# Optimization experiments

Hardware: AMD Instinct MI355X
Metric: run time of the kernel (lower is better)

Reference implementation:

```python
import jax, jax.numpy as jnp
import numpy as np

B, H, W, C, NH = 4, 64, 64, 512, 16
HD = C // NH
BIAS_LEVEL = 0.1
LN_EPS = 1e-5


def layernorm(x, g, b):
    m = jnp.mean(x, axis=-1, keepdims=True)
    v = jnp.mean(jnp.square(x - m), axis=-1, keepdims=True)
    return (x - m) * jax.lax.rsqrt(v + LN_EPS) * g + b


def partition(x, idx):
    # x: [B, L, C] -> windows [nW, S, C]
    xg = x.reshape(B, H, W, C)
    if idx == 0:  # horizontal strips: window = one row of length W
        return xg.reshape(B * H, W, C)
    else:  # vertical strips: window = one column of length H, ordered by column
        return xg.transpose(0, 2, 1, 3).reshape(B * W, H, C)


def unpartition(w, idx):
    # w: [nW, S, C] -> [B, L, C]
    if idx == 0:
        return w.reshape(B, H * W, C)
    else:
        return w.reshape(B, W, H, C).transpose(0, 2, 1, 3).reshape(B, H * W, C)


def eg_attention(q, k, v, res_x, rpe, idx):
    # q,k,v: [B, L, C]; res_x: [B, L, C]; rpe: [1, NH, S, S]
    S = rpe.shape[-1]
    nW = (B * H * W) // S

    def to_heads(t):
        return partition(t, idx).reshape(nW, S, NH, HD).transpose(0, 2, 1, 3)

    qh, kh, vh = to_heads(q), to_heads(k), to_heads(v)  # [nW, NH, S, HD]
    attn = jnp.einsum('whsd,whtd->whst', qh, kh) + BIAS_LEVEL * rpe
    # gating mask from raw scores
    M = jnp.mean(jnp.abs(attn), axis=(1, 2, 3), keepdims=True)  # [nW,1,1,1]
    M = M / jnp.max(M)
    M = jnp.maximum(M, 0.5)
    # L2-normalize rows, trig transform
    norm = jnp.sqrt(jnp.sum(jnp.square(attn), axis=-1, keepdims=True))
    attn = attn / jnp.maximum(norm, 1e-12)
    attn = 1.0 - jnp.cos(attn * (jnp.pi / 2))
    attn = attn * M
    out = jnp.einsum('whst,whtd->whsd', attn, vh)  # [nW, NH, S, HD]
    out = out.transpose(0, 2, 1, 3).reshape(nW, S, C)
    out = unpartition(out, idx)  # [B, L, C]
    # masked residual: res_x is chunked sequentially (row-major), as in the source
    res = res_x.reshape(nW, S, C) * (1.0 - M[:, 0])
    res = res.reshape(B, H * W, C)
    return out + res


def eg_block(x, rpe, idx, ln1_g, ln1_b, wqkv, wproj, bproj, ln2_g, ln2_b,
             wfc1, bfc1, wfc2, bfc2):
    img = layernorm(x, ln1_g, ln1_b)
    qkv = img @ wqkv  # [B, L, 3C]
    q, k, v = jnp.split(qkv, 3, axis=-1)
    att = eg_attention(q, k, v, x, rpe, idx)
    att = att @ wproj + bproj
    x = x + att
    h = layernorm(x, ln2_g, ln2_b)
    h = jax.nn.gelu(h @ wfc1 + bfc1, approximate=False) @ wfc2 + bfc2
    return x + h


def setup_inputs() -> dict:
    key = jax.random.key(0)
    ks = jax.random.split(key, 16)
    d = {
        'x': jax.random.normal(ks[0], (B, H * W, C), jnp.float32),
        'rpe0': jax.random.normal(ks[1], (1, NH, W, W), jnp.float32),
        'rpe1': jax.random.normal(ks[2], (1, NH, H, H), jnp.float32),
    }
    for i, blk in enumerate(['0', '1']):
        kk = jax.random.split(ks[3 + i], 8)
        d['ln1_g' + blk] = jnp.ones((C,), jnp.float32)
        d['ln1_b' + blk] = jnp.zeros((C,), jnp.float32)
        d['wqkv' + blk] = jax.random.normal(kk[0], (C, 3 * C), jnp.float32) * 0.02
        d['wproj' + blk] = jax.random.normal(kk[1], (C, C), jnp.float32) * 0.02
        d['bproj' + blk] = jnp.zeros((C,), jnp.float32)
        d['ln2_g' + blk] = jnp.ones((C,), jnp.float32)
        d['ln2_b' + blk] = jnp.zeros((C,), jnp.float32)
        d['wfc1_' + blk] = jax.random.normal(kk[2], (C, 4 * C), jnp.float32) * 0.02
        d['bfc1_' + blk] = jnp.zeros((4 * C,), jnp.float32)
        d['wfc2_' + blk] = jax.random.normal(kk[3], (4 * C, C), jnp.float32) * 0.02
        d['bfc2_' + blk] = jnp.zeros((C,), jnp.float32)
    return d


def reference(x, rpe0, rpe1,
              ln1_g0, ln1_b0, wqkv0, wproj0, bproj0, ln2_g0, ln2_b0,
              wfc1_0, bfc1_0, wfc2_0, bfc2_0,
              ln1_g1, ln1_b1, wqkv1, wproj1, bproj1, ln2_g1, ln2_b1,
              wfc1_1, bfc1_1, wfc2_1, bfc2_1):
    x = eg_block(x, rpe0, 0, ln1_g0, ln1_b0, wqkv0, wproj0, bproj0,
                 ln2_g0, ln2_b0, wfc1_0, bfc1_0, wfc2_0, bfc2_0)
    x = eg_block(x, rpe1, 1, ln1_g1, ln1_b1, wqkv1, wproj1, bproj1,
                 ln2_g1, ln2_b1, wfc1_1, bfc1_1, wfc2_1, bfc2_1)
    return x
```

## Files before the change

### kernel.cpp

```cpp
#include <hip/hip_runtime.h>
#include <cstdint>
#include <cstddef>

typedef __bf16 bf16;
typedef __attribute__((ext_vector_type(4))) float f32x4;
typedef __attribute__((ext_vector_type(8))) __bf16 bf16x8;
typedef __attribute__((ext_vector_type(4))) __bf16 bf16x4;

static __device__ __forceinline__ f32x4 mfma16(bf16x8 a, bf16x8 b, f32x4 c) {
    return __builtin_amdgcn_mfma_f32_16x16x32_bf16(a, b, c, 0, 0, 0);
}

#define GLOAD_LDS16(gsrc, ldst)                                              \
    __builtin_amdgcn_global_load_lds(                                        \
        (const __attribute__((address_space(1))) void*)(gsrc),               \
        (__attribute__((address_space(3))) void*)(ldst), 16, 0, 0)

static __device__ __forceinline__ float fast_gelu(float x) {
    const float xs = x * 0.70710678118f;
    const float a  = fabsf(xs);
    const float t  = 1.0f / fmaf(0.3275911f, a, 1.0f);
    float p = fmaf(t, 1.061405429f, -1.453152027f);
    p = fmaf(t, p, 1.421413741f);
    p = fmaf(t, p, -0.284496736f);
    p = fmaf(t, p, 0.254829592f);
    const float erfa = 1.0f - p * t * __expf(-a * a);
    const float erfx = (xs < 0.f) ? -erfa : erfa;
    return 0.5f * x * (1.0f + erfx);
}

__global__ __launch_bounds__(256)
void transpose_cast(const float* __restrict__ W, bf16* __restrict__ Wt, int K, int N) {
    __shared__ float tile[32][33];
    const int n0 = blockIdx.x * 32, k0 = blockIdx.y * 32;
    const int tx = threadIdx.x & 31, ty = threadIdx.x >> 5;
    #pragma unroll
    for (int i = ty; i < 32; i += 8)
        tile[i][tx] = W[(size_t)(k0 + i) * N + n0 + tx];
    __syncthreads();
    #pragma unroll
    for (int i = ty; i < 32; i += 8)
        Wt[(size_t)(n0 + i) * K + k0 + tx] = (bf16)tile[tx][i];
}

__global__ __launch_bounds__(256)
void ln_kernel(const float* __restrict__ x, const float* __restrict__ g,
               const float* __restrict__ b, bf16* __restrict__ out) {
    const int row = blockIdx.x * 4 + (threadIdx.x >> 6);
    const int lane = threadIdx.x & 63;
    const float* p = x + (size_t)row * 512 + lane * 8;
    const float4 a0 = *(const float4*)p;
    const float4 a1 = *(const float4*)(p + 4);
    float vx[8] = {a0.x, a0.y, a0.z, a0.w, a1.x, a1.y, a1.z, a1.w};
    float s = 0.f, ss = 0.f;
    #pragma unroll
    for (int k = 0; k < 8; ++k) { s += vx[k]; ss += vx[k] * vx[k]; }
    #pragma unroll
    for (int m = 1; m < 64; m <<= 1) {
        s  += __shfl_xor(s, m);
        ss += __shfl_xor(ss, m);
    }
    const float mean = s * (1.0f / 512.0f);
    const float var  = ss * (1.0f / 512.0f) - mean * mean;
    const float inv  = rsqrtf(var + 1e-5f);
    const int c0 = lane * 8;
    const float4 g0 = *(const float4*)&g[c0], g1 = *(const float4*)&g[c0 + 4];
    const float4 b0 = *(const float4*)&b[c0], b1 = *(const float4*)&b[c0 + 4];
    const float gv[8] = {g0.x, g0.y, g0.z, g0.w, g1.x, g1.y, g1.z, g1.w};
    const float bv[8] = {b0.x, b0.y, b0.z, b0.w, b1.x, b1.y, b1.z, b1.w};
    bf16x8 o;
    #pragma unroll
    for (int k = 0; k < 8; ++k)
        o[k] = (bf16)((vx[k] - mean) * inv * gv[k] + bv[k]);
    *(bf16x8*)&out[(size_t)row * 512 + c0] = o;
}

template <int EPI>
__global__ __launch_bounds__(256)
void gemm_bt(const bf16* __restrict__ A, const bf16* __restrict__ Bt,
             int N, int K, const float* __restrict__ bias,
             const float* __restrict__ res, float* __restrict__ outf,
             bf16* __restrict__ outh) {
    __shared__ __align__(16) bf16 lsA[2][128 * 32];
    __shared__ __align__(16) bf16 lsB[2][128 * 32];
    const int nx = gridDim.x;
    const int nwg = nx * gridDim.y;
    const int flat = blockIdx.y * nx + blockIdx.x;
    const int cpx = nwg >> 3;
    const int bswz = (flat & 7) * cpx + (flat >> 3);
    const int bn = bswz % nx, bm = bswz / nx;

    const int tid = threadIdx.x, lane = tid & 63, wv = tid >> 6;
    const int wm = (wv & 1) * 64, wn = (wv >> 1) * 64;
    const int l15 = lane & 15, lg = lane >> 4;
    const size_t abase = (size_t)bm * 128 * K;
    const size_t bbase = (size_t)bn * 128 * K;
    const int srow = lane >> 2;
    const int slot = lane & 3;
    const int r0 = (wv * 2 + 0) * 16 + srow;
    const int r1 = (wv * 2 + 1) * 16 + srow;
    const int ks0 = (slot ^ ((r0 >> 1) & 3)) * 8;
    const int ks1 = (slot ^ ((r1 >> 1) & 3)) * 8;

    f32x4 acc[4][4] = {};

    auto stage = [&](int buf, int kt) {
        GLOAD_LDS16(&A[abase + (size_t)r0 * K + kt + ks0],
                    &lsA[buf][(wv * 2 + 0) * 512]);
        GLOAD_LDS16(&A[abase + (size_t)r1 * K + kt + ks1],
                    &lsA[buf][(wv * 2 + 1) * 512]);
        GLOAD_LDS16(&Bt[bbase + (size_t)r0 * K + kt + ks0],
                    &lsB[buf][(wv * 2 + 0) * 512]);
        GLOAD_LDS16(&Bt[bbase + (size_t)r1 * K + kt + ks1],
                    &lsB[buf][(wv * 2 + 1) * 512]);
    };
    auto compute = [&](int buf) {
        bf16x8 af[4], bfr[4];
        #pragma unroll
        for (int i = 0; i < 4; ++i) {
            const int r = wm + i * 16 + l15;
            af[i] = *(const bf16x8*)
                &lsA[buf][r * 32 + ((lg ^ ((r >> 1) & 3)) * 8)];
        }
        #pragma unroll
        for (int j = 0; j < 4; ++j) {
            const int r = wn + j * 16 + l15;
            bfr[j] = *(const bf16x8*)
                &lsB[buf][r * 32 + ((lg ^ ((r >> 1) & 3)) * 8)];
        }
        #pragma unroll
        for (int i = 0; i < 4; ++i)
            #pragma unroll
            for (int j = 0; j < 4; ++j)
                acc[i][j] = mfma16(af[i], bfr[j], acc[i][j]);
    };

    const int NK = K >> 5;
    stage(0, 0);
    __syncthreads();
    int cur = 0;
    for (int t = 0; t < NK - 1; ++t) {
        stage(cur ^ 1, (t + 1) * 32);
        compute(cur);
        __syncthreads();
        cur ^= 1;
    }
    compute(cur);

    #pragma unroll
    for (int i = 0; i < 4; ++i) {
        #pragma unroll
        for (int r = 0; r < 4; ++r) {
            const size_t row = (size_t)bm * 128 + wm + i * 16 + lg * 4 + r;
            #pragma unroll
            for (int j = 0; j < 4; ++j) {
                const int col = bn * 128 + wn + j * 16 + l15;
                const float v = acc[i][j][r];
                if constexpr (EPI == 0) {
                    outh[row * N + col] = (bf16)v;
                } else if constexpr (EPI == 1) {
                    outf[row * N + col] = v + bias[col] + res[row * N + col];
                } else {
                    outh[row * N + col] = (bf16)fast_gelu(v + bias[col]);
                }
            }
        }
    }
}

__global__ __launch_bounds__(256)
void attn_stats(const bf16* __restrict__ qkv, const float* __restrict__ rpe,
                float* __restrict__ Mraw4, int idx) {
    __shared__ float lsum[4];
    const int bid = blockIdx.x;
    const int w = bid >> 2;
    const int tid = threadIdx.x, lane = tid & 63, wv = tid >> 6;
    const int h = (bid & 3) * 4 + wv;
    const int l15 = lane & 15, lg = lane >> 4;
    const long gbase = (idx == 0) ? (long)w * 64 : ((long)(w >> 6) * 4096 + (w & 63));
    const long gstride = (idx == 0) ? 1 : 64;
    bf16x8 kf[4];
    #pragma unroll
    for (int i = 0; i < 4; ++i) {
        const long gs = gbase + (long)(i * 16 + l15) * gstride;
        kf[i] = *(const bf16x8*)&qkv[gs * 1536 + 512 + h * 32 + lg * 8];
    }
    const float* rh = rpe + h * 4096;
    float asum = 0.f;
    #pragma unroll
    for (int mi = 0; mi < 4; ++mi) {
        const long gs = gbase + (long)(mi * 16 + l15) * gstride;
        const bf16x8 qf = *(const bf16x8*)&qkv[gs * 1536 + h * 32 + lg * 8];
        f32x4 sc[4] = {};
        #pragma unroll
        for (int ni = 0; ni < 4; ++ni) sc[ni] = mfma16(qf, kf[ni], sc[ni]);
        #pragma unroll
        for (int r = 0; r < 4; ++r) {
            const int srow = mi * 16 + lg * 4 + r;
            #pragma unroll
            for (int ni = 0; ni < 4; ++ni)
                asum += fabsf(sc[ni][r] + 0.1f * rh[srow * 64 + ni * 16 + l15]);
        }
    }
    #pragma unroll
    for (int m = 1; m < 64; m <<= 1) asum += __shfl_xor(asum, m);
    if (lane == 0) lsum[wv] = asum;
    __syncthreads();
    if (tid == 0) Mraw4[bid] = lsum[0] + lsum[1] + lsum[2] + lsum[3];
}

__global__ __launch_bounds__(256)
void mcalc(const float* __restrict__ Mraw4, float* __restrict__ Mv) {
    __shared__ float red[4];
    const int t = threadIdx.x, lane = t & 63;
    const float v = (Mraw4[t * 4] + Mraw4[t * 4 + 1] + Mraw4[t * 4 + 2] +
                     Mraw4[t * 4 + 3]) * (1.0f / 65536.0f);
    float m = v;
    #pragma unroll
    for (int msk = 1; msk < 64; msk <<= 1) m = fmaxf(m, __shfl_xor(m, msk));
    if (lane == 0) red[t >> 6] = m;
    __syncthreads();
    const float mm = fmaxf(fmaxf(red[0], red[1]), fmaxf(red[2], red[3]));
    Mv[t] = fmaxf(v / mm, 0.5f);
}

__global__ __launch_bounds__(256)
void attn_apply(const bf16* __restrict__ qkv, const float* __restrict__ rpe,
                const float* __restrict__ Mv, const float* __restrict__ xin,
                bf16* __restrict__ attout, int idx) {
    __shared__ __align__(16) bf16 lsP[4][64 * 64];
    __shared__ __align__(16) bf16 lsVt[4][32 * 64];
    const int bid = blockIdx.x;
    const int w = bid >> 2;
    const int tid = threadIdx.x, lane = tid & 63, wv = tid >> 6;
    const int h = (bid & 3) * 4 + wv;
    const int l15 = lane & 15, lg = lane >> 4;
    const long gbase = (idx == 0) ? (long)w * 64 : ((long)(w >> 6) * 4096 + (w & 63));
    const long gstride = (idx == 0) ? 1 : 64;
    const float Mw = Mv[w];
    bf16* P  = lsP[wv];
    bf16* Vt = lsVt[wv];

    {
        const int d4 = (lane & 7) * 4;
        #pragma unroll
        for (int it = 0; it < 8; ++it) {
            const int t = it * 8 + (lane >> 3);
            const bf16x4 v = *(const bf16x4*)
                &qkv[(gbase + (long)t * gstride) * 1536 + 1024 + h * 32 + d4];
            #pragma unroll
            for (int e = 0; e < 4; ++e) {
                const int d = d4 + e;
                Vt[d * 64 + (t ^ ((d & 7) * 8))] = v[e];
            }
        }
    }
    bf16x8 kf[4];
    #pragma unroll
    for (int i = 0; i < 4; ++i) {
        const long gs = gbase + (long)(i * 16 + l15) * gstride;
        kf[i] = *(const bf16x8*)&qkv[gs * 1536 + 512 + h * 32 + lg * 8];
    }
    const float* rh = rpe + h * 4096;
    #pragma unroll
    for (int mi = 0; mi < 4; ++mi) {
        const long gs = gbase + (long)(mi * 16 + l15) * gstride;
        const bf16x8 qf = *(const bf16x8*)&qkv[gs * 1536 + h * 32 + lg * 8];
        f32x4 sc[4] = {};
        #pragma unroll
        for (int ni = 0; ni < 4; ++ni) sc[ni] = mfma16(qf, kf[ni], sc[ni]);
        #pragma unroll
        for (int r = 0; r < 4; ++r) {
            const int srow = mi * 16 + lg * 4 + r;
            float vv[4], ssq = 0.f;
            #pragma unroll
            for (int ni = 0; ni < 4; ++ni) {
                const float v = sc[ni][r] + 0.1f * rh[srow * 64 + ni * 16 + l15];
                vv[ni] = v;
                ssq += v * v;
            }
            ssq += __shfl_xor(ssq, 1);
            ssq += __shfl_xor(ssq, 2);
            ssq += __shfl_xor(ssq, 4);
            ssq += __shfl_xor(ssq, 8);
            const float is = 1.0f / fmaxf(sqrtf(ssq), 1e-12f);
            #pragma unroll
            for (int ni = 0; ni < 4; ++ni) {
                const float v = (1.0f - __cosf(vv[ni] * is * 1.57079632679f)) * Mw;
                const int col = ni * 16 + l15;
                P[srow * 64 + (col ^ ((srow & 7) * 8))] = (bf16)v;
            }
        }
    }
    f32x4 acc[4][2] = {};
    #pragma unroll
    for (int kk = 0; kk < 2; ++kk) {
        bf16x8 bfr[2];
        #pragma unroll
        for (int dj = 0; dj < 2; ++dj) {
            const int d = dj * 16 + l15;
            bfr[dj] = *(const bf16x8*)&Vt[d * 64 + ((kk * 32 + lg * 8) ^ ((d & 7) * 8))];
        }
        #pragma unroll
        for (int mi = 0; mi < 4; ++mi) {
            const int s = mi * 16 + l15;
            const bf16x8 af = *(const bf16x8*)&P[s * 64 + ((kk * 32 + lg * 8) ^ ((s & 7) * 8))];
            #pragma unroll
            for (int dj = 0; dj < 2; ++dj)
                acc[mi][dj] = mfma16(af, bfr[dj], acc[mi][dj]);
        }
    }
    #pragma unroll
    for (int mi = 0; mi < 4; ++mi) {
        #pragma unroll
        for (int r = 0; r < 4; ++r) {
            const int s = mi * 16 + lg * 4 + r;
            const long gg = gbase + (long)s * gstride;
            const float rm = 1.0f - Mv[(int)(gg >> 6)];
            #pragma unroll
            for (int dj = 0; dj < 2; ++dj) {
                const int d = dj * 16 + l15;
                const size_t oidx = (size_t)gg * 512 + h * 32 + d;
                attout[oidx] = (bf16)(acc[mi][dj][r] + xin[oidx] * rm);
            }
        }
    }
}

extern "C" void kernel_launch(void* const* d_in, const int* in_sizes, int n_in,
                              void* d_out, int out_size, void* d_ws, size_t ws_size,
                              hipStream_t stream) {
    const float* x    = (const float*)d_in[0];
    const float* rpe0 = (const float*)d_in[1];
    const float* rpe1 = (const float*)d_in[2];
    auto W = [&](int i) { return (const float*)d_in[i]; };

    char* ws = (char*)d_ws;
    size_t off = 0;
    auto alloc = [&](size_t bytes) {
        void* p = ws + off;
        off += (bytes + 255) & ~(size_t)255;
        return p;
    };
    bf16 *wqkvT[2], *wprojT[2], *wfc1T[2], *wfc2T[2];
    for (int b = 0; b < 2; ++b) {
        wqkvT[b] = (bf16*)alloc((size_t)1536 * 512 * 2);
        wprojT[b] = (bf16*)alloc((size_t)512 * 512 * 2);
        wfc1T[b] = (bf16*)alloc((size_t)2048 * 512 * 2);
        wfc2T[b] = (bf16*)alloc((size_t)512 * 2048 * 2);
    }
    bf16* IMG = (bf16*)alloc((size_t)16384 * 512 * 2);
    bf16* QKV = (bf16*)alloc((size_t)16384 * 1536 * 2);
    bf16* ATT = (bf16*)alloc((size_t)16384 * 512 * 2);
    bf16* H1  = QKV;
    float* X1    = (float*)alloc((size_t)16384 * 512 * 4);
    float* Mraw4 = (float*)alloc(1024 * 4);
    float* Mv    = (float*)alloc(256 * 4);
    float* XMID  = (float*)d_out;

    auto launchT = [&](const float* Wp, bf16* Wt, int K, int N) {
        transpose_cast<<<dim3(N / 32, K / 32), 256, 0, stream>>>(Wp, Wt, K, N);
    };
    launchT(W(5), wqkvT[0], 512, 1536);
    launchT(W(6), wprojT[0], 512, 512);
    launchT(W(10), wfc1T[0], 512, 2048);
    launchT(W(12), wfc2T[0], 2048, 512);
    launchT(W(16), wqkvT[1], 512, 1536);
    launchT(W(17), wprojT[1], 512, 512);
    launchT(W(21), wfc1T[1], 512, 2048);
    launchT(W(23), wfc2T[1], 2048, 512);

    for (int b = 0; b < 2; ++b) {
        const float* xin = (b == 0) ? x : X1;
        const float* rpe = (b == 0) ? rpe0 : rpe1;
        const int base = (b == 0) ? 3 : 14;
        const float* ln1g = W(base + 0);
        const float* ln1b = W(base + 1);
        const float* bproj = W(base + 4);
        const float* ln2g = W(base + 5);
        const float* ln2b = W(base + 6);
        const float* bfc1 = W(base + 8);
        const float* bfc2 = W(base + 10);

        ln_kernel<<<4096, 256, 0, stream>>>(xin, ln1g, ln1b, IMG);
        gemm_bt<0><<<dim3(12, 128), 256, 0, stream>>>(
            IMG, wqkvT[b], 1536, 512, nullptr, nullptr, nullptr, QKV);
        attn_stats<<<1024, 256, 0, stream>>>(QKV, rpe, Mraw4, b);
        mcalc<<<1, 256, 0, stream>>>(Mraw4, Mv);
        attn_apply<<<1024, 256, 0, stream>>>(QKV, rpe, Mv, xin, ATT, b);
        gemm_bt<1><<<dim3(4, 128), 256, 0, stream>>>(
            ATT, wprojT[b], 512, 512, bproj, xin, XMID, nullptr);
        ln_kernel<<<4096, 256, 0, stream>>>(XMID, ln2g, ln2b, IMG);
        gemm_bt<2><<<dim3(16, 128), 256, 0, stream>>>(
            IMG, wfc1T[b], 2048, 512, bfc1, nullptr, nullptr, H1);
        gemm_bt<1><<<dim3(4, 128), 256, 0, stream>>>(
            H1, wfc2T[b], 512, 2048, bfc2, XMID, (b == 0) ? X1 : XMID, nullptr);
    }
    (void)in_sizes; (void)n_in; (void)out_size; (void)ws_size;
}
```

Before: 506.3 us.

## Add 256x256-tile 8-wave GEMM with interleaved LDS staging for QKV and FC1

```diff
diff --git a/kernel.cpp b/kernel.cpp
--- a/kernel.cpp
+++ b/kernel.cpp
@@ -15,6 +15,13 @@
     __builtin_amdgcn_global_load_lds(                                        \
         (const __attribute__((address_space(1))) void*)(gsrc),               \
         (__attribute__((address_space(3))) void*)(ldst), 16, 0, 0)
+
+#define WAITVM(N) asm volatile("s_waitcnt vmcnt(" #N ")" ::: "memory")
+#define PHASE_BAR()                                                          \
+    do {                                                                     \
+        __builtin_amdgcn_sched_barrier(0);                                   \
+        __builtin_amdgcn_s_barrier();                                        \
+    } while (0)
 
 static __device__ __forceinline__ float fast_gelu(float x) {
     const float xs = x * 0.70710678118f;
@@ -76,11 +83,143 @@
 }
 
 template <int EPI>
+__global__ __launch_bounds__(512, 2)
+void gemm256(const bf16* __restrict__ A, const bf16* __restrict__ Bt,
+             int N, int K, const float* __restrict__ bias,
+             bf16* __restrict__ outh) {
+    __shared__ __align__(16) bf16 lsA[2][256 * 64];
+    __shared__ __align__(16) bf16 lsB[2][256 * 64];
+    const int nx = gridDim.x, nwg = nx * gridDim.y;
+    const int flat = blockIdx.y * nx + blockIdx.x;
+    const int cpx = nwg >> 3;
+    const int bswz = (flat & 7) * cpx + (flat >> 3);
+    const int bn = bswz % nx, bm = bswz / nx;
+
+    const int tid = threadIdx.x, lane = tid & 63, wv = tid >> 6;
+    const int wr = wv >> 2, wc = wv & 3;
+    const int l15 = lane & 15, lg = lane >> 4;
+
+    const size_t abase = (size_t)bm * 256 * K;
+    const size_t bbase = (size_t)bn * 256 * K;
+
+    const int st_r8 = lane >> 3;
+    const int st_sg = (lane & 7) ^ st_r8;
+
+    auto stageA = [&](int buf, int h, int kt) {
+        #pragma unroll
+        for (int rr = 0; rr < 2; ++rr) {
+            const int rowbase = (h * 2 + rr) * 64 + wv * 8;
+            GLOAD_LDS16(&A[abase + (size_t)(rowbase + st_r8) * K + kt + st_sg * 8],
+                        &lsA[buf][rowbase * 64]);
+        }
+    };
+    auto stageB = [&](int buf, int h, int kt) {
+        #pragma unroll
+        for (int rr = 0; rr < 2; ++rr) {
+            const int rowbase = (h * 2 + rr) * 64 + wv * 8;
+            GLOAD_LDS16(&Bt[bbase + (size_t)(rowbase + st_r8) * K + kt + st_sg * 8],
+                        &lsB[buf][rowbase * 64]);
+        }
+    };
+
+    const int r7 = l15 & 7;
+    const int aoff0 = (wr * 128 + l15) * 64 + ((0 + lg) ^ r7) * 8;
+    const int aoff1 = (wr * 128 + l15) * 64 + ((4 + lg) ^ r7) * 8;
+    const int boff0 = (wc * 64 + l15) * 64 + ((0 + lg) ^ r7) * 8;
+    const int boff1 = (wc * 64 + l15) * 64 + ((4 + lg) ^ r7) * 8;
+
+    f32x4 acc[8][4] = {};
+    bf16x8 bfrag[4][2], afrag[2][2];
+
+    auto readB = [&](int buf) {
+        #pragma unroll
+        for (int n = 0; n < 4; ++n) {
+            bfrag[n][0] = *(const bf16x8*)&lsB[buf][boff0 + n * 1024];
+            bfrag[n][1] = *(const bf16x8*)&lsB[buf][boff1 + n * 1024];
+        }
+    };
+    auto readA = [&](int buf, int mq) {
+        #pragma unroll
+        for (int mm = 0; mm < 2; ++mm) {
+            afrag[mm][0] = *(const bf16x8*)&lsA[buf][aoff0 + (mq * 2 + mm) * 1024];
+            afrag[mm][1] = *(const bf16x8*)&lsA[buf][aoff1 + (mq * 2 + mm) * 1024];
+        }
+    };
+    auto mfma_quad = [&](int mq) {
+        __builtin_amdgcn_s_setprio(1);
+        #pragma unroll
+        for (int kk = 0; kk < 2; ++kk)
+            #pragma unroll
+            for (int mm = 0; mm < 2; ++mm)
+                #pragma unroll
+                for (int n = 0; n < 4; ++n)
+                    acc[mq * 2 + mm][n] =
+                        mfma16(afrag[mm][kk], bfrag[n][kk], acc[mq * 2 + mm][n]);
+        __builtin_amdgcn_s_setprio(0);
+    };
+
+    const int NT = K >> 6;
+    stageA(0, 0, 0); stageB(0, 0, 0); stageA(0, 1, 0); stageB(0, 1, 0);
+    stageB(1, 0, 64); stageB(1, 1, 64);
+    WAITVM(4);
+    PHASE_BAR();
+
+    for (int t = 0; t < NT; t += 2) {
+        const int kt2 = (t + 2) * 64, kt3 = (t + 3) * 64;
+        const bool pf = (t + 3) < NT;
+        readB(0); readA(0, 0);
+        stageA(1, 0, (t + 1) * 64); stageA(1, 1, (t + 1) * 64);
+        PHASE_BAR(); mfma_quad(0); PHASE_BAR();
+        readA(0, 1);
+        if (pf) stageB(0, 0, kt2);
+        PHASE_BAR(); mfma_quad(1); PHASE_BAR();
+        readA(0, 2);
+        if (pf) stageB(0, 1, kt2);
+        PHASE_BAR(); mfma_quad(2); PHASE_BAR();
+        readA(0, 3);
+        PHASE_BAR(); mfma_quad(3);
+        if (pf) { WAITVM(4); } else { WAITVM(0); }
+        PHASE_BAR();
+        readB(1); readA(1, 0);
+        if (pf) { stageA(0, 0, kt2); stageA(0, 1, kt2); }
+        PHASE_BAR(); mfma_quad(0); PHASE_BAR();
+        readA(1, 1);
+        if (pf) stageB(1, 0, kt3);
+        PHASE_BAR(); mfma_quad(1); PHASE_BAR();
+        readA(1, 2);
+        if (pf) stageB(1, 1, kt3);
+        PHASE_BAR(); mfma_quad(2); PHASE_BAR();
+        readA(1, 3);
+        PHASE_BAR(); mfma_quad(3);
+        if (pf) WAITVM(4);
+        PHASE_BAR();
+    }
+
+    const int orow0 = bm * 256 + wr * 128;
+    const int ocol0 = bn * 256 + wc * 64;
+    #pragma unroll
+    for (int m = 0; m < 8; ++m) {
+        #pragma unroll
+        for (int q = 0; q < 4; ++q) {
+            const size_t row = orow0 + m * 16 + lg * 4 + q;
+            #pragma unroll
+            for (int n = 0; n < 4; ++n) {
+                const int col = ocol0 + n * 16 + l15;
+                const float v = acc[m][n][q];
+                if constexpr (EPI == 0) {
+                    outh[row * N + col] = (bf16)v;
+                } else {
+                    outh[row * N + col] = (bf16)fast_gelu(v + bias[col]);
+                }
+            }
+        }
+    }
+}
+
 __global__ __launch_bounds__(256)
 void gemm_bt(const bf16* __restrict__ A, const bf16* __restrict__ Bt,
              int N, int K, const float* __restrict__ bias,
-             const float* __restrict__ res, float* __restrict__ outf,
-             bf16* __restrict__ outh) {
+             const float* __restrict__ res, float* __restrict__ outf) {
     __shared__ __align__(16) bf16 lsA[2][128 * 32];
     __shared__ __align__(16) bf16 lsB[2][128 * 32];
     const int nx = gridDim.x;
@@ -155,14 +294,7 @@
             #pragma unroll
             for (int j = 0; j < 4; ++j) {
                 const int col = bn * 128 + wn + j * 16 + l15;
-                const float v = acc[i][j][r];
-                if constexpr (EPI == 0) {
-                    outh[row * N + col] = (bf16)v;
-                } else if constexpr (EPI == 1) {
-                    outf[row * N + col] = v + bias[col] + res[row * N + col];
-                } else {
-                    outh[row * N + col] = (bf16)fast_gelu(v + bias[col]);
-                }
+                outf[row * N + col] = acc[i][j][r] + bias[col] + res[row * N + col];
             }
         }
     }
@@ -383,18 +515,18 @@
         const float* bfc2 = W(base + 10);
 
         ln_kernel<<<4096, 256, 0, stream>>>(xin, ln1g, ln1b, IMG);
-        gemm_bt<0><<<dim3(12, 128), 256, 0, stream>>>(
-            IMG, wqkvT[b], 1536, 512, nullptr, nullptr, nullptr, QKV);
+        gemm256<0><<<dim3(6, 64), 512, 0, stream>>>(
+            IMG, wqkvT[b], 1536, 512, nullptr, QKV);
         attn_stats<<<1024, 256, 0, stream>>>(QKV, rpe, Mraw4, b);
         mcalc<<<1, 256, 0, stream>>>(Mraw4, Mv);
         attn_apply<<<1024, 256, 0, stream>>>(QKV, rpe, Mv, xin, ATT, b);
-        gemm_bt<1><<<dim3(4, 128), 256, 0, stream>>>(
-            ATT, wprojT[b], 512, 512, bproj, xin, XMID, nullptr);
+        gemm_bt<<<dim3(4, 128), 256, 0, stream>>>(
+            ATT, wprojT[b], 512, 512, bproj, xin, XMID);
         ln_kernel<<<4096, 256, 0, stream>>>(XMID, ln2g, ln2b, IMG);
-        gemm_bt<2><<<dim3(16, 128), 256, 0, stream>>>(
-            IMG, wfc1T[b], 2048, 512, bfc1, nullptr, nullptr, H1);
-        gemm_bt<1><<<dim3(4, 128), 256, 0, stream>>>(
-            H1, wfc2T[b], 512, 2048, bfc2, XMID, (b == 0) ? X1 : XMID, nullptr);
+        gemm256<2><<<dim3(8, 64), 512, 0, stream>>>(
+            IMG, wfc1T[b], 2048, 512, bfc1, H1);
+        gemm_bt<<<dim3(4, 128), 256, 0, stream>>>(
+            H1, wfc2T[b], 512, 2048, bfc2, XMID, (b == 0) ? X1 : XMID);
     }
     (void)in_sizes; (void)n_in; (void)out_size; (void)ws_size;
 }
```

Result: slower. 516.7 us (+2.1%).
